# Performance work log

Hardware: AMD Instinct MI355X
Metric: run time of the kernel (lower is better)

Reference implementation:

```python
import jax, jax.numpy as jnp
import numpy as np

BLOCK_SIZE = 64
WINDOW_SIZE = 256  # local_window pattern: each query block attends to blocks within the window
NEG_INF = -1e30


def setup_inputs() -> dict:
    key = jax.random.key(0)
    kq, kk, kv = jax.random.split(key, 3)
    B, S, H, D = 2, 4096, 16, 64
    q = jax.random.normal(kq, (B, S, H, D), dtype=jnp.float32)
    k = jax.random.normal(kk, (B, S, H, D), dtype=jnp.float32)
    v = jax.random.normal(kv, (B, S, H, D), dtype=jnp.float32)
    return {"q": q, "k": k, "v": v}


def _block_sparse_attn(q, k, v):
    # q, k, v: [B, S, H, D]
    B, S, H, D = q.shape
    bs = BLOCK_SIZE
    N = S // bs                      # number of blocks
    W = WINDOW_SIZE // bs            # window in blocks (4)
    half = W // 2
    offsets = jnp.arange(-half, half + 1)          # [K] neighbor offsets, K = W+1 = 5
    K = offsets.shape[0]

    i = jnp.arange(N)
    j = i[:, None] + offsets[None, :]              # [N, K] neighbor block ids
    valid = (j >= 0) & (j < N)                     # boundary mask
    jc = jnp.clip(j, 0, N - 1)

    # reshape into blocks: [B, H, N, bs, D]
    qb = q.reshape(B, N, bs, H, D).transpose(0, 3, 1, 2, 4)
    kb = k.reshape(B, N, bs, H, D).transpose(0, 3, 1, 2, 4)
    vb = v.reshape(B, N, bs, H, D).transpose(0, 3, 1, 2, 4)

    # gather only the active (neighbor) key/value blocks: [B, H, N, K, bs, D]
    kn = kb[:, :, jc]
    vn = vb[:, :, jc]

    scale = 1.0 / jnp.sqrt(jnp.asarray(D, dtype=q.dtype))
    # block scores: [B, H, N, bs, K, bs]
    scores = jnp.einsum('bhnqd,bhnkcd->bhnqkc', qb, kn) * scale
    scores = jnp.where(valid[None, None, :, None, :, None], scores, NEG_INF)

    # softmax over the union of active key blocks for each query block
    scores = scores.reshape(B, H, N, bs, K * bs)
    attn = jax.nn.softmax(scores, axis=-1)
    out = jnp.einsum('bhnqe,bhned->bhnqd', attn, vn.reshape(B, H, N, K * bs, D))

    # back to [B, S, H, D]
    return out.transpose(0, 2, 3, 1, 4).reshape(B, S, H, D)


def reference(q, k, v):
    return _block_sparse_attn(q, k, v)
```

## Files before the change

kernel.cpp:

```cpp
#include <hip/hip_runtime.h>

#define S_DIM 4096
#define H_DIM 16
#define D_DIM 64
#define N_BLK 64
#define PITCH 72
#define NEG_INF_F (-1e30f)

typedef __attribute__((ext_vector_type(4))) float f32x4;
typedef __attribute__((ext_vector_type(8))) short s16x8;
typedef __attribute__((ext_vector_type(4))) short s16x4;

__device__ __forceinline__ short f2bf(float f) {
    unsigned int u = __builtin_bit_cast(unsigned int, f);
    unsigned int r = (u + 0x7fffu + ((u >> 16) & 1u)) >> 16;
    return (short)r;
}

__global__ __launch_bounds__(256) void bsattn_kernel(
    const float* __restrict__ qg, const float* __restrict__ kg,
    const float* __restrict__ vg, float* __restrict__ outg)
{
    __shared__ short lds_k [N_BLK * PITCH];
    __shared__ short lds_vt[D_DIM * PITCH];
    __shared__ short lds_p [4 * 64 * PITCH];

    const int tid  = threadIdx.x;
    const int w    = tid >> 6;
    const int lane = tid & 63;
    const int quad = lane >> 4;
    const int l16  = lane & 15;

    const int b  = blockIdx.z;
    const int h  = blockIdx.y;
    const int n0 = blockIdx.x << 2;
    const int n  = n0 + w;

    s16x8 aq[4][2];
#pragma unroll
    for (int rt = 0; rt < 4; ++rt) {
        const size_t qrow = ((size_t)(b * S_DIM + n * 64 + rt * 16 + l16) * H_DIM + h) * D_DIM;
#pragma unroll
        for (int c = 0; c < 2; ++c) {
            const float4* qp = reinterpret_cast<const float4*>(qg + qrow + c * 32 + quad * 8);
            float4 f0 = qp[0];
            float4 f1 = qp[1];
            s16x8 a;
            a[0] = f2bf(f0.x * 0.125f); a[1] = f2bf(f0.y * 0.125f);
            a[2] = f2bf(f0.z * 0.125f); a[3] = f2bf(f0.w * 0.125f);
            a[4] = f2bf(f1.x * 0.125f); a[5] = f2bf(f1.y * 0.125f);
            a[6] = f2bf(f1.z * 0.125f); a[7] = f2bf(f1.w * 0.125f);
            aq[rt][c] = a;
        }
    }

    f32x4 o[4][4];
    float m_run[4][4], l_run[4][4];
#pragma unroll
    for (int rt = 0; rt < 4; ++rt) {
#pragma unroll
        for (int t = 0; t < 4; ++t) o[rt][t] = (f32x4){0.f, 0.f, 0.f, 0.f};
#pragma unroll
        for (int r = 0; r < 4; ++r) { m_run[rt][r] = NEG_INF_F; l_run[rt][r] = 0.f; }
    }

    const int tr = tid >> 2;
    const int d0 = (tid & 3) << 4;

    short* const myp = lds_p + w * (64 * PITCH);

    for (int ji = 0; ji < 8; ++ji) {
        const int j = n0 - 2 + ji;
        __syncthreads();
        if (j >= 0 && j < N_BLK) {
            const size_t src = ((size_t)(b * S_DIM + j * 64 + tr) * H_DIM + h) * D_DIM + d0;
            const float4* kp = reinterpret_cast<const float4*>(kg + src);
            const float4* vp = reinterpret_cast<const float4*>(vg + src);
            float4 k0 = kp[0], k1 = kp[1], k2 = kp[2], k3 = kp[3];
            float4 v0 = vp[0], v1 = vp[1], v2 = vp[2], v3 = vp[3];
            short* kd = lds_k + tr * PITCH + d0;
            s16x4 w0 = {f2bf(k0.x), f2bf(k0.y), f2bf(k0.z), f2bf(k0.w)};
            s16x4 w1 = {f2bf(k1.x), f2bf(k1.y), f2bf(k1.z), f2bf(k1.w)};
            s16x4 w2 = {f2bf(k2.x), f2bf(k2.y), f2bf(k2.z), f2bf(k2.w)};
            s16x4 w3 = {f2bf(k3.x), f2bf(k3.y), f2bf(k3.z), f2bf(k3.w)};
            *reinterpret_cast<s16x4*>(kd)      = w0;
            *reinterpret_cast<s16x4*>(kd + 4)  = w1;
            *reinterpret_cast<s16x4*>(kd + 8)  = w2;
            *reinterpret_cast<s16x4*>(kd + 12) = w3;
            float vf[16] = {v0.x, v0.y, v0.z, v0.w, v1.x, v1.y, v1.z, v1.w,
                            v2.x, v2.y, v2.z, v2.w, v3.x, v3.y, v3.z, v3.w};
#pragma unroll
            for (int i = 0; i < 16; ++i)
                lds_vt[(d0 + i) * PITCH + tr] = f2bf(vf[i]);
        }
        __syncthreads();

        if (j < 0 || j >= N_BLK) continue;
        const int rel = j - n;
        if (rel < -2 || rel > 2) continue;

#pragma unroll
        for (int rt = 0; rt < 4; ++rt) {
            f32x4 s[4];
#pragma unroll
            for (int t = 0; t < 4; ++t) {
                const short* kb = lds_k + (t * 16 + l16) * PITCH + quad * 8;
                s16x8 b0 = *reinterpret_cast<const s16x8*>(kb);
                s16x8 b1 = *reinterpret_cast<const s16x8*>(kb + 32);
                f32x4 acc = {0.f, 0.f, 0.f, 0.f};
                acc = __builtin_amdgcn_mfma_f32_16x16x32_bf16(aq[rt][0], b0, acc, 0, 0, 0);
                acc = __builtin_amdgcn_mfma_f32_16x16x32_bf16(aq[rt][1], b1, acc, 0, 0, 0);
                s[t] = acc;
            }
            float mnew[4], alpha[4];
#pragma unroll
            for (int r = 0; r < 4; ++r) {
                float mx = fmaxf(fmaxf(s[0][r], s[1][r]), fmaxf(s[2][r], s[3][r]));
                mx = fmaxf(mx, __shfl_xor(mx, 1, 16));
                mx = fmaxf(mx, __shfl_xor(mx, 2, 16));
                mx = fmaxf(mx, __shfl_xor(mx, 4, 16));
                mx = fmaxf(mx, __shfl_xor(mx, 8, 16));
                const float mn = fmaxf(m_run[rt][r], mx);
                alpha[r] = __expf(m_run[rt][r] - mn);
                m_run[rt][r] = mn;
                mnew[r] = mn;
            }
#pragma unroll
            for (int t = 0; t < 4; ++t)
#pragma unroll
                for (int r = 0; r < 4; ++r) s[t][r] = __expf(s[t][r] - mnew[r]);
#pragma unroll
            for (int r = 0; r < 4; ++r) {
                float rs = s[0][r] + s[1][r] + s[2][r] + s[3][r];
                rs += __shfl_xor(rs, 1, 16);
                rs += __shfl_xor(rs, 2, 16);
                rs += __shfl_xor(rs, 4, 16);
                rs += __shfl_xor(rs, 8, 16);
                l_run[rt][r] = l_run[rt][r] * alpha[r] + rs;
#pragma unroll
                for (int t = 0; t < 4; ++t) o[rt][t][r] *= alpha[r];
            }
#pragma unroll
            for (int t = 0; t < 4; ++t)
#pragma unroll
                for (int r = 0; r < 4; ++r)
                    myp[(rt * 16 + quad * 4 + r) * PITCH + t * 16 + l16] = f2bf(s[t][r]);
        }

        asm volatile("s_waitcnt lgkmcnt(0)" ::: "memory");

#pragma unroll
        for (int rt = 0; rt < 4; ++rt) {
            const short* pr = myp + (rt * 16 + l16) * PITCH + quad * 8;
            s16x8 pa0 = *reinterpret_cast<const s16x8*>(pr);
            s16x8 pa1 = *reinterpret_cast<const s16x8*>(pr + 32);
#pragma unroll
            for (int t = 0; t < 4; ++t) {
                const short* vb = lds_vt + (t * 16 + l16) * PITCH + quad * 8;
                s16x8 b0 = *reinterpret_cast<const s16x8*>(vb);
                s16x8 b1 = *reinterpret_cast<const s16x8*>(vb + 32);
                o[rt][t] = __builtin_amdgcn_mfma_f32_16x16x32_bf16(pa0, b0, o[rt][t], 0, 0, 0);
                o[rt][t] = __builtin_amdgcn_mfma_f32_16x16x32_bf16(pa1, b1, o[rt][t], 0, 0, 0);
            }
        }
    }

#pragma unroll
    for (int rt = 0; rt < 4; ++rt) {
#pragma unroll
        for (int r = 0; r < 4; ++r) {
            const float inv = 1.0f / l_run[rt][r];
            float* op = outg +
                ((size_t)(b * S_DIM + n * 64 + rt * 16 + quad * 4 + r) * H_DIM + h) * D_DIM + l16;
#pragma unroll
            for (int t = 0; t < 4; ++t)
                op[t * 16] = o[rt][t][r] * inv;
        }
    }
}

extern "C" void kernel_launch(void* const* d_in, const int* in_sizes, int n_in,
                              void* d_out, int out_size, void* d_ws, size_t ws_size,
                              hipStream_t stream) {
    const float* q = (const float*)d_in[0];
    const float* k = (const float*)d_in[1];
    const float* v = (const float*)d_in[2];
    float* out = (float*)d_out;
    const int B = in_sizes[0] / (S_DIM * H_DIM * D_DIM);
    dim3 grid(N_BLK / 4, H_DIM, B);
    dim3 block(256);
    hipLaunchKernelGGL(bsattn_kernel, grid, block, 0, stream, q, k, v, out);
}
```

Measured before the change: 180.1 us.

## Compute transposed S=K·Q^T to keep P in registers, halve query blocks per workgroup

The QK^T MFMA is computed with K as the A operand so the score tile comes out transposed. Softmax probabilities can then be packed straight into the B-operand layout for the PV MFMA, which removes the per-wave LDS staging buffer for P and its wait. Each workgroup now covers 2 query blocks (two waves of 32 rows each) instead of 4, so the grid doubles and the K/V loop drops from 8 to 6 blocks. This raises the redundant K/V loads per query block. BF16 conversion switches to a cheaper perm-based round-half-up, with launch bounds set for 4 blocks per CU.

```diff
diff --git a/kernel.cpp b/kernel.cpp
--- a/kernel.cpp
+++ b/kernel.cpp
@@ -6,24 +6,30 @@
 #define N_BLK 64
 #define PITCH 72
 #define NEG_INF_F (-1e30f)
+#define QSCALE 0.125f
 
 typedef __attribute__((ext_vector_type(4))) float f32x4;
 typedef __attribute__((ext_vector_type(8))) short s16x8;
 typedef __attribute__((ext_vector_type(4))) short s16x4;
-
-__device__ __forceinline__ short f2bf(float f) {
-    unsigned int u = __builtin_bit_cast(unsigned int, f);
-    unsigned int r = (u + 0x7fffu + ((u >> 16) & 1u)) >> 16;
-    return (short)r;
-}
-
-__global__ __launch_bounds__(256) void bsattn_kernel(
+typedef __attribute__((ext_vector_type(4))) unsigned int u32x4;
+typedef __attribute__((ext_vector_type(2))) unsigned int u32x2;
+
+__device__ __forceinline__ unsigned int fbits(float f) {
+    return __builtin_bit_cast(unsigned int, f);
+}
+__device__ __forceinline__ unsigned int pkbf(float a, float b) {
+    return __builtin_amdgcn_perm(fbits(b) + 0x8000u, fbits(a) + 0x8000u, 0x07060302u);
+}
+__device__ __forceinline__ short f2bf1(float f) {
+    return (short)((fbits(f) + 0x8000u) >> 16);
+}
+
+__global__ __launch_bounds__(256, 4) void bsattn_kernel(
     const float* __restrict__ qg, const float* __restrict__ kg,
     const float* __restrict__ vg, float* __restrict__ outg)
 {
     __shared__ short lds_k [N_BLK * PITCH];
     __shared__ short lds_vt[D_DIM * PITCH];
-    __shared__ short lds_p [4 * 64 * PITCH];
 
     const int tid  = threadIdx.x;
     const int w    = tid >> 6;
@@ -33,43 +39,41 @@
 
     const int b  = blockIdx.z;
     const int h  = blockIdx.y;
-    const int n0 = blockIdx.x << 2;
-    const int n  = n0 + w;
-
-    s16x8 aq[4][2];
-#pragma unroll
-    for (int rt = 0; rt < 4; ++rt) {
-        const size_t qrow = ((size_t)(b * S_DIM + n * 64 + rt * 16 + l16) * H_DIM + h) * D_DIM;
-#pragma unroll
-        for (int c = 0; c < 2; ++c) {
-            const float4* qp = reinterpret_cast<const float4*>(qg + qrow + c * 32 + quad * 8);
+    const int n0 = blockIdx.x << 1;
+    const int n  = n0 + (w >> 1);
+    const int qrow0 = n * 64 + (w & 1) * 32;
+
+    s16x8 bq[2][2];
+#pragma unroll
+    for (int qt = 0; qt < 2; ++qt) {
+        const size_t qrow = ((size_t)(b * S_DIM + qrow0 + qt * 16 + l16) * H_DIM + h) * D_DIM;
+#pragma unroll
+        for (int hh = 0; hh < 2; ++hh) {
+            const float4* qp = reinterpret_cast<const float4*>(qg + qrow + hh * 32 + quad * 8);
             float4 f0 = qp[0];
             float4 f1 = qp[1];
-            s16x8 a;
-            a[0] = f2bf(f0.x * 0.125f); a[1] = f2bf(f0.y * 0.125f);
-            a[2] = f2bf(f0.z * 0.125f); a[3] = f2bf(f0.w * 0.125f);
-            a[4] = f2bf(f1.x * 0.125f); a[5] = f2bf(f1.y * 0.125f);
-            a[6] = f2bf(f1.z * 0.125f); a[7] = f2bf(f1.w * 0.125f);
-            aq[rt][c] = a;
-        }
-    }
-
-    f32x4 o[4][4];
-    float m_run[4][4], l_run[4][4];
-#pragma unroll
-    for (int rt = 0; rt < 4; ++rt) {
-#pragma unroll
-        for (int t = 0; t < 4; ++t) o[rt][t] = (f32x4){0.f, 0.f, 0.f, 0.f};
-#pragma unroll
-        for (int r = 0; r < 4; ++r) { m_run[rt][r] = NEG_INF_F; l_run[rt][r] = 0.f; }
+            u32x4 u;
+            u.x = pkbf(f0.x * QSCALE, f0.y * QSCALE);
+            u.y = pkbf(f0.z * QSCALE, f0.w * QSCALE);
+            u.z = pkbf(f1.x * QSCALE, f1.y * QSCALE);
+            u.w = pkbf(f1.z * QSCALE, f1.w * QSCALE);
+            bq[qt][hh] = __builtin_bit_cast(s16x8, u);
+        }
+    }
+
+    f32x4 o[2][4];
+    float m_run[2], l_run[2];
+#pragma unroll
+    for (int qt = 0; qt < 2; ++qt) {
+        m_run[qt] = NEG_INF_F; l_run[qt] = 0.f;
+#pragma unroll
+        for (int dt = 0; dt < 4; ++dt) o[qt][dt] = (f32x4){0.f, 0.f, 0.f, 0.f};
     }
 
     const int tr = tid >> 2;
     const int d0 = (tid & 3) << 4;
 
-    short* const myp = lds_p + w * (64 * PITCH);
-
-    for (int ji = 0; ji < 8; ++ji) {
+    for (int ji = 0; ji < 6; ++ji) {
         const int j = n0 - 2 + ji;
         __syncthreads();
         if (j >= 0 && j < N_BLK) {
@@ -79,19 +83,19 @@
             float4 k0 = kp[0], k1 = kp[1], k2 = kp[2], k3 = kp[3];
             float4 v0 = vp[0], v1 = vp[1], v2 = vp[2], v3 = vp[3];
             short* kd = lds_k + tr * PITCH + d0;
-            s16x4 w0 = {f2bf(k0.x), f2bf(k0.y), f2bf(k0.z), f2bf(k0.w)};
-            s16x4 w1 = {f2bf(k1.x), f2bf(k1.y), f2bf(k1.z), f2bf(k1.w)};
-            s16x4 w2 = {f2bf(k2.x), f2bf(k2.y), f2bf(k2.z), f2bf(k2.w)};
-            s16x4 w3 = {f2bf(k3.x), f2bf(k3.y), f2bf(k3.z), f2bf(k3.w)};
-            *reinterpret_cast<s16x4*>(kd)      = w0;
-            *reinterpret_cast<s16x4*>(kd + 4)  = w1;
-            *reinterpret_cast<s16x4*>(kd + 8)  = w2;
-            *reinterpret_cast<s16x4*>(kd + 12) = w3;
+            u32x2 ka = {pkbf(k0.x, k0.y), pkbf(k0.z, k0.w)};
+            u32x2 kb = {pkbf(k1.x, k1.y), pkbf(k1.z, k1.w)};
+            u32x2 kc = {pkbf(k2.x, k2.y), pkbf(k2.z, k2.w)};
+            u32x2 ke = {pkbf(k3.x, k3.y), pkbf(k3.z, k3.w)};
+            *reinterpret_cast<u32x2*>(kd)      = ka;
+            *reinterpret_cast<u32x2*>(kd + 4)  = kb;
+            *reinterpret_cast<u32x2*>(kd + 8)  = kc;
+            *reinterpret_cast<u32x2*>(kd + 12) = ke;
             float vf[16] = {v0.x, v0.y, v0.z, v0.w, v1.x, v1.y, v1.z, v1.w,
                             v2.x, v2.y, v2.z, v2.w, v3.x, v3.y, v3.z, v3.w};
 #pragma unroll
             for (int i = 0; i < 16; ++i)
-                lds_vt[(d0 + i) * PITCH + tr] = f2bf(vf[i]);
+                lds_vt[(d0 + i) * PITCH + tr] = f2bf1(vf[i]);
         }
         __syncthreads();
 
@@ -99,82 +103,90 @@
         const int rel = j - n;
         if (rel < -2 || rel > 2) continue;
 
-#pragma unroll
-        for (int rt = 0; rt < 4; ++rt) {
-            f32x4 s[4];
-#pragma unroll
-            for (int t = 0; t < 4; ++t) {
-                const short* kb = lds_k + (t * 16 + l16) * PITCH + quad * 8;
-                s16x8 b0 = *reinterpret_cast<const s16x8*>(kb);
-                s16x8 b1 = *reinterpret_cast<const s16x8*>(kb + 32);
-                f32x4 acc = {0.f, 0.f, 0.f, 0.f};
-                acc = __builtin_amdgcn_mfma_f32_16x16x32_bf16(aq[rt][0], b0, acc, 0, 0, 0);
-                acc = __builtin_amdgcn_mfma_f32_16x16x32_bf16(aq[rt][1], b1, acc, 0, 0, 0);
-                s[t] = acc;
+        f32x4 sa[2][4];
+#pragma unroll
+        for (int kt = 0; kt < 4; ++kt) {
+            const short* kbp = lds_k + (kt * 16 + l16) * PITCH + quad * 8;
+            s16x8 kf0 = *reinterpret_cast<const s16x8*>(kbp);
+            s16x8 kf1 = *reinterpret_cast<const s16x8*>(kbp + 32);
+            f32x4 z = {0.f, 0.f, 0.f, 0.f};
+            f32x4 a0 = __builtin_amdgcn_mfma_f32_16x16x32_bf16(kf0, bq[0][0], z, 0, 0, 0);
+            sa[0][kt] = __builtin_amdgcn_mfma_f32_16x16x32_bf16(kf1, bq[0][1], a0, 0, 0, 0);
+            f32x4 a1 = __builtin_amdgcn_mfma_f32_16x16x32_bf16(kf0, bq[1][0], z, 0, 0, 0);
+            sa[1][kt] = __builtin_amdgcn_mfma_f32_16x16x32_bf16(kf1, bq[1][1], a1, 0, 0, 0);
+        }
+
+        s16x8 pa[2][2];
+#pragma unroll
+        for (int qt = 0; qt < 2; ++qt) {
+            float mx = NEG_INF_F;
+#pragma unroll
+            for (int kt = 0; kt < 4; ++kt)
+#pragma unroll
+                for (int r = 0; r < 4; ++r) mx = fmaxf(mx, sa[qt][kt][r]);
+            mx = fmaxf(mx, __shfl_xor(mx, 16));
+            mx = fmaxf(mx, __shfl_xor(mx, 32));
+            const float mn = fmaxf(m_run[qt], mx);
+            const float alpha = __expf(m_run[qt] - mn);
+            m_run[qt] = mn;
+
+            float rs = 0.f;
+            unsigned int pk[4][2];
+#pragma unroll
+            for (int kt = 0; kt < 4; ++kt) {
+                float e0 = __expf(sa[qt][kt][0] - mn);
+                float e1 = __expf(sa[qt][kt][1] - mn);
+                float e2 = __expf(sa[qt][kt][2] - mn);
+                float e3 = __expf(sa[qt][kt][3] - mn);
+                rs += (e0 + e1) + (e2 + e3);
+                pk[kt][0] = pkbf(e0, e1);
+                pk[kt][1] = pkbf(e2, e3);
             }
-            float mnew[4], alpha[4];
-#pragma unroll
-            for (int r = 0; r < 4; ++r) {
-                float mx = fmaxf(fmaxf(s[0][r], s[1][r]), fmaxf(s[2][r], s[3][r]));
-                mx = fmaxf(mx, __shfl_xor(mx, 1, 16));
-                mx = fmaxf(mx, __shfl_xor(mx, 2, 16));
-                mx = fmaxf(mx, __shfl_xor(mx, 4, 16));
-                mx = fmaxf(mx, __shfl_xor(mx, 8, 16));
-                const float mn = fmaxf(m_run[rt][r], mx);
-                alpha[r] = __expf(m_run[rt][r] - mn);
-                m_run[rt][r] = mn;
-                mnew[r] = mn;
+            rs += __shfl_xor(rs, 16);
+            rs += __shfl_xor(rs, 32);
+            l_run[qt] = l_run[qt] * alpha + rs;
+
+            float ab[4];
+#pragma unroll
+            for (int r = 0; r < 4; ++r)
+                ab[r] = __shfl(alpha, (lane & 48) + quad * 4 + r);
+#pragma unroll
+            for (int dt = 0; dt < 4; ++dt)
+#pragma unroll
+                for (int r = 0; r < 4; ++r) o[qt][dt][r] *= ab[r];
+
+            pa[qt][0] = __builtin_bit_cast(s16x8, (u32x4){pk[0][0], pk[0][1], pk[1][0], pk[1][1]});
+            pa[qt][1] = __builtin_bit_cast(s16x8, (u32x4){pk[2][0], pk[2][1], pk[3][0], pk[3][1]});
+        }
+
+#pragma unroll
+        for (int dt = 0; dt < 4; ++dt) {
+            const short* vb = lds_vt + (dt * 16 + l16) * PITCH + quad * 4;
+            s16x4 v00 = *reinterpret_cast<const s16x4*>(vb);
+            s16x4 v01 = *reinterpret_cast<const s16x4*>(vb + 16);
+            s16x4 v10 = *reinterpret_cast<const s16x4*>(vb + 32);
+            s16x4 v11 = *reinterpret_cast<const s16x4*>(vb + 48);
+            s16x8 vf0 = {v00[0], v00[1], v00[2], v00[3], v01[0], v01[1], v01[2], v01[3]};
+            s16x8 vf1 = {v10[0], v10[1], v10[2], v10[3], v11[0], v11[1], v11[2], v11[3]};
+#pragma unroll
+            for (int qt = 0; qt < 2; ++qt) {
+                o[qt][dt] = __builtin_amdgcn_mfma_f32_16x16x32_bf16(pa[qt][0], vf0, o[qt][dt], 0, 0, 0);
+                o[qt][dt] = __builtin_amdgcn_mfma_f32_16x16x32_bf16(pa[qt][1], vf1, o[qt][dt], 0, 0, 0);
             }
-#pragma unroll
-            for (int t = 0; t < 4; ++t)
-#pragma unroll
-                for (int r = 0; r < 4; ++r) s[t][r] = __expf(s[t][r] - mnew[r]);
-#pragma unroll
-            for (int r = 0; r < 4; ++r) {
-                float rs = s[0][r] + s[1][r] + s[2][r] + s[3][r];
-                rs += __shfl_xor(rs, 1, 16);
-                rs += __shfl_xor(rs, 2, 16);
-                rs += __shfl_xor(rs, 4, 16);
-                rs += __shfl_xor(rs, 8, 16);
-                l_run[rt][r] = l_run[rt][r] * alpha[r] + rs;
-#pragma unroll
-                for (int t = 0; t < 4; ++t) o[rt][t][r] *= alpha[r];
-            }
-#pragma unroll
-            for (int t = 0; t < 4; ++t)
-#pragma unroll
-                for (int r = 0; r < 4; ++r)
-                    myp[(rt * 16 + quad * 4 + r) * PITCH + t * 16 + l16] = f2bf(s[t][r]);
-        }
-
-        asm volatile("s_waitcnt lgkmcnt(0)" ::: "memory");
-
-#pragma unroll
-        for (int rt = 0; rt < 4; ++rt) {
-            const short* pr = myp + (rt * 16 + l16) * PITCH + quad * 8;
-            s16x8 pa0 = *reinterpret_cast<const s16x8*>(pr);
-            s16x8 pa1 = *reinterpret_cast<const s16x8*>(pr + 32);
-#pragma unroll
-            for (int t = 0; t < 4; ++t) {
-                const short* vb = lds_vt + (t * 16 + l16) * PITCH + quad * 8;
-                s16x8 b0 = *reinterpret_cast<const s16x8*>(vb);
-                s16x8 b1 = *reinterpret_cast<const s16x8*>(vb + 32);
-                o[rt][t] = __builtin_amdgcn_mfma_f32_16x16x32_bf16(pa0, b0, o[rt][t], 0, 0, 0);
-                o[rt][t] = __builtin_amdgcn_mfma_f32_16x16x32_bf16(pa1, b1, o[rt][t], 0, 0, 0);
-            }
-        }
-    }
-
-#pragma unroll
-    for (int rt = 0; rt < 4; ++rt) {
+        }
+    }
+
+#pragma unroll
+    for (int qt = 0; qt < 2; ++qt) {
 #pragma unroll
         for (int r = 0; r < 4; ++r) {
-            const float inv = 1.0f / l_run[rt][r];
-            float* op = outg +
-                ((size_t)(b * S_DIM + n * 64 + rt * 16 + quad * 4 + r) * H_DIM + h) * D_DIM + l16;
-#pragma unroll
-            for (int t = 0; t < 4; ++t)
-                op[t * 16] = o[rt][t][r] * inv;
+            const float lb = __shfl(l_run[qt], (lane & 48) + quad * 4 + r);
+            const float inv = 1.0f / lb;
+            const int row = qrow0 + qt * 16 + quad * 4 + r;
+            float* op = outg + ((size_t)(b * S_DIM + row) * H_DIM + h) * D_DIM + l16;
+#pragma unroll
+            for (int dt = 0; dt < 4; ++dt)
+                op[dt * 16] = o[qt][dt][r] * inv;
         }
     }
 }
@@ -187,7 +199,7 @@
     const float* v = (const float*)d_in[2];
     float* out = (float*)d_out;
     const int B = in_sizes[0] / (S_DIM * H_DIM * D_DIM);
-    dim3 grid(N_BLK / 4, H_DIM, B);
+    dim3 grid(N_BLK / 2, H_DIM, B);
     dim3 block(256);
     hipLaunchKernelGGL(bsattn_kernel, grid, block, 0, stream, q, k, v, out);
 }
```

Measured after the change: 161.8 us. -10.1%, faster.
